# Performance work log

Hardware: AMD Instinct MI355X
Metric: run time of the kernel (lower is better)

## Reference

```python
import jax, jax.numpy as jnp
import numpy as np

B, S, D, H, L, F, V = 8, 4096, 1024, 16, 6, 2048, 256
DH = D // H

def _pe(seq, dim):
    pos = jnp.arange(seq, dtype=jnp.float32)[:, None]
    div = jnp.exp(jnp.arange(0, dim, 2, dtype=jnp.float32) * (-np.log(10000.0) / dim))
    pe = jnp.zeros((seq, dim), jnp.float32)
    pe = pe.at[:, 0::2].set(jnp.sin(pos * div))
    pe = pe.at[:, 1::2].set(jnp.cos(pos * div))
    return pe

def _ln(x, w, b):
    m = x.mean(-1, keepdims=True)
    v = ((x - m) ** 2).mean(-1, keepdims=True)
    return (x - m) * jax.lax.rsqrt(v + 1e-5) * w + b

def setup_inputs():
    key = jax.random.key(0)
    ks = jax.random.split(key, 8)
    s = 0.02
    return {
        'tgt': jax.random.normal(ks[0], (B, S, D), jnp.float32),
        'in_proj_w': jax.random.normal(ks[1], (L, 3 * D, D), jnp.float32) * s,
        'in_proj_b': jnp.zeros((L, 3 * D), jnp.float32),
        'out_proj_w': jax.random.normal(ks[2], (L, D, D), jnp.float32) * s,
        'out_proj_b': jnp.zeros((L, D), jnp.float32),
        'ln1_w': jnp.ones((L, D), jnp.float32), 'ln1_b': jnp.zeros((L, D), jnp.float32),
        'lin1_w': jax.random.normal(ks[3], (L, F, D), jnp.float32) * s,
        'lin1_b': jnp.zeros((L, F), jnp.float32),
        'lin2_w': jax.random.normal(ks[4], (L, D, F), jnp.float32) * s,
        'lin2_b': jnp.zeros((L, D), jnp.float32),
        'ln2_w': jnp.ones((L, D), jnp.float32), 'ln2_b': jnp.zeros((L, D), jnp.float32),
        'w_out': jax.random.normal(ks[5], (V, D), jnp.float32) * s,
        'b_out': jnp.zeros((V,), jnp.float32),
    }

def reference(tgt, in_proj_w, in_proj_b, out_proj_w, out_proj_b, ln1_w, ln1_b,
              lin1_w, lin1_b, lin2_w, lin2_b, ln2_w, ln2_b, w_out, b_out):
    # eval-mode cached decode step of CachedDecoderOnly.forward (dropout inactive)
    out = tgt + _pe(S, D)[None]  # [B,S,D]
    for i in range(L):
        q = out[:, -1:, :]  # query is only the last token
        wq, wk, wv = jnp.split(in_proj_w[i], 3, axis=0)
        bq, bk, bv = jnp.split(in_proj_b[i], 3)
        Q = (q @ wq.T + bq).reshape(B, 1, H, DH)
        K = (out @ wk.T + bk).reshape(B, -1, H, DH)
        Vv = (out @ wv.T + bv).reshape(B, -1, H, DH)
        sc = jnp.einsum('bqhd,bkhd->bhqk', Q, K) / jnp.sqrt(jnp.float32(DH))
        a = jax.nn.softmax(sc, axis=-1)
        o = jnp.einsum('bhqk,bkhd->bqhd', a, Vv).reshape(B, 1, D)
        o = o @ out_proj_w[i].T + out_proj_b[i]
        y = _ln(q + o, ln1_w[i], ln1_b[i])
        ff = jax.nn.relu(y @ lin1_w[i].T + lin1_b[i]) @ lin2_w[i].T + lin2_b[i]
        out = _ln(y + ff, ln2_w[i], ln2_b[i])  # [B,1,D] -> src for next layer
    return out @ w_out.T + b_out  # [B,1,V]
```

## Files before the change

### kernel.cpp

```cpp
#include <hip/hip_runtime.h>
#include <hip/hip_bf16.h>

#define BB 8
#define SS 4096
#define DD 1024
#define HH 16
#define LL 6
#define FF 2048
#define VV 256
#define NC 32

typedef __attribute__((ext_vector_type(8))) short bf16x8;
typedef __attribute__((ext_vector_type(4))) float f32x4;

__device__ __forceinline__ unsigned short f2bf(float f) {
    union { float f; unsigned u; } v; v.f = f;
    unsigned r = v.u + 0x7FFFu + ((v.u >> 16) & 1u);
    return (unsigned short)(r >> 16);
}

__global__ __launch_bounds__(256) void pe_kernel(float* __restrict__ pe) {
    int s = blockIdx.x;
    float fs = (float)s;
    for (int i = threadIdx.x; i < DD / 2; i += 256) {
        float div = expf((-logf(10000.0f) / (float)DD) * (float)(2 * i));
        float a = fs * div;
        pe[(long)s * DD + 2 * i]     = sinf(a);
        pe[(long)s * DD + 2 * i + 1] = cosf(a);
    }
}

template <int K, int RELU, int MODE>
__global__ __launch_bounds__(256) void gemm8k(
    const float* __restrict__ A, long sA,
    const float* __restrict__ A2, long sA2,
    const float* __restrict__ W,
    const float* __restrict__ bias,
    const float* __restrict__ R1, long sR1,
    const float* __restrict__ R2, long sR2,
    const float* __restrict__ lnw, const float* __restrict__ lnb,
    const float* __restrict__ lnsrc,
    float* __restrict__ C, int N)
{
    int wave = threadIdx.x >> 6, lane = threadIdx.x & 63;
    int n = blockIdx.x * 4 + wave;
    if (n >= N) return;

    float mean[8], rstd[8];
    if (MODE != 0) {
        const float* S = (MODE == 1) ? A : lnsrc;
        long ss = (MODE == 1) ? sA : 1024L;
        const int SK = (MODE == 1) ? K : 1024;
        #pragma unroll
        for (int m = 0; m < 8; ++m) {
            float s1 = 0.f, s2 = 0.f;
            const float4* Sr = reinterpret_cast<const float4*>(S + (long)m * ss);
            #pragma unroll
            for (int k4 = 0; k4 < SK / 256; ++k4) {
                float4 a = Sr[k4 * 64 + lane];
                s1 += a.x + a.y + a.z + a.w;
                s2 += a.x * a.x + a.y * a.y + a.z * a.z + a.w * a.w;
            }
            for (int off = 32; off; off >>= 1) {
                s1 += __shfl_xor(s1, off, 64);
                s2 += __shfl_xor(s2, off, 64);
            }
            float mu = s1 / (float)SK;
            mean[m] = mu;
            rstd[m] = rsqrtf(s2 / (float)SK - mu * mu + 1e-5f);
        }
    }

    float acc[8] = {0.f,0.f,0.f,0.f,0.f,0.f,0.f,0.f};
    const float4* W4 = reinterpret_cast<const float4*>(W + (long)n * K);
    float4 wv[K / 256];
    #pragma unroll
    for (int kb = 0; kb < K / 256; ++kb) wv[kb] = W4[kb * 64 + lane];
    #pragma unroll
    for (int kb = 0; kb < K / 256; ++kb) {
        int k4 = kb * 64 + lane;
        float4 w = wv[kb];
        float4 lw, lb;
        if (MODE == 1) {
            lw = reinterpret_cast<const float4*>(lnw)[k4];
            lb = reinterpret_cast<const float4*>(lnb)[k4];
        }
        #pragma unroll
        for (int m = 0; m < 8; ++m) {
            float4 a = reinterpret_cast<const float4*>(A + (long)m * sA)[k4];
            if (A2) {
                float4 a2 = reinterpret_cast<const float4*>(A2 + (long)m * sA2)[k4];
                a.x += a2.x; a.y += a2.y; a.z += a2.z; a.w += a2.w;
            }
            if (MODE == 1) {
                float mu = mean[m], rs = rstd[m];
                a.x = (a.x - mu) * rs * lw.x + lb.x;
                a.y = (a.y - mu) * rs * lw.y + lb.y;
                a.z = (a.z - mu) * rs * lw.z + lb.z;
                a.w = (a.w - mu) * rs * lw.w + lb.w;
            }
            acc[m] += a.x * w.x + a.y * w.y + a.z * w.z + a.w * w.w;
        }
    }
    #pragma unroll
    for (int m = 0; m < 8; ++m)
        for (int off = 32; off; off >>= 1) acc[m] += __shfl_xor(acc[m], off, 64);
    if (lane == 0) {
        float bs = bias ? bias[n] : 0.f;
        #pragma unroll
        for (int m = 0; m < 8; ++m) {
            float v = acc[m] + bs;
            if (MODE == 0) {
                if (R1) v += R1[(long)m * sR1 + n];
                if (R2) v += R2[(long)m * sR2 + n];
            }
            if (MODE == 2)
                v += (lnsrc[(long)m * 1024 + n] - mean[m]) * rstd[m] * lnw[n] + lnb[n];
            if (RELU) v = fmaxf(v, 0.f);
            C[(long)m * N + n] = v;
        }
    }
}

__global__ __launch_bounds__(256) void u_kernel(const float* __restrict__ Q,
                                                const float* __restrict__ wk,
                                                unsigned short* __restrict__ ub)
{
    int h = blockIdx.y;
    int e = blockIdx.x * 256 + threadIdx.x;
    __shared__ float qs[8][64];
    for (int idx = threadIdx.x; idx < 512; idx += 256) {
        int b = idx >> 6, d = idx & 63;
        qs[b][d] = Q[(long)b * DD + h * 64 + d];
    }
    __syncthreads();
    float acc[8] = {0.f,0.f,0.f,0.f,0.f,0.f,0.f,0.f};
    for (int d = 0; d < 64; ++d) {
        float wv = wk[(long)(h * 64 + d) * DD + e];
        #pragma unroll
        for (int b = 0; b < 8; ++b) acc[b] += qs[b][d] * wv;
    }
    #pragma unroll
    for (int b = 0; b < 8; ++b)
        ub[((long)(b * HH + h)) * DD + e] = f2bf(acc[b]);
}

__global__ __launch_bounds__(512) void attn_kernel(
    const float* __restrict__ tgt, const float* __restrict__ pe,
    const unsigned short* __restrict__ ub,
    float* __restrict__ ctxp, float* __restrict__ ml)
{
    int sc = blockIdx.x, b = blockIdx.y;
    int wave = threadIdx.x >> 6, lane = threadIdx.x & 63;
    int q = lane >> 4, n = lane & 15;
    __shared__ float scs[16][128];
    __shared__ unsigned short P[16 * 128];

    int s0 = sc * 128;

    {
        int s = s0 + wave * 16 + n;
        const float* xrow = tgt + ((long)b * SS + s) * DD;
        const float* prow = pe + (long)s * DD;
        const unsigned short* urow = ub + ((long)(b * HH) + n) * DD;
        f32x4 acc = {0.f, 0.f, 0.f, 0.f};
        #pragma unroll 4
        for (int ks = 0; ks < 32; ++ks) {
            int e0 = ks * 32 + q * 8;
            bf16x8 a = *reinterpret_cast<const bf16x8*>(urow + e0);
            float4 x0 = *reinterpret_cast<const float4*>(xrow + e0);
            float4 x1 = *reinterpret_cast<const float4*>(xrow + e0 + 4);
            float4 p0 = *reinterpret_cast<const float4*>(prow + e0);
            float4 p1 = *reinterpret_cast<const float4*>(prow + e0 + 4);
            union { short sh[8]; bf16x8 v; } bu;
            bu.sh[0] = (short)f2bf(x0.x + p0.x);
            bu.sh[1] = (short)f2bf(x0.y + p0.y);
            bu.sh[2] = (short)f2bf(x0.z + p0.z);
            bu.sh[3] = (short)f2bf(x0.w + p0.w);
            bu.sh[4] = (short)f2bf(x1.x + p1.x);
            bu.sh[5] = (short)f2bf(x1.y + p1.y);
            bu.sh[6] = (short)f2bf(x1.z + p1.z);
            bu.sh[7] = (short)f2bf(x1.w + p1.w);
            acc = __builtin_amdgcn_mfma_f32_16x16x32_bf16(a, bu.v, acc, 0, 0, 0);
        }
        #pragma unroll
        for (int r = 0; r < 4; ++r) scs[q * 4 + r][wave * 16 + n] = acc[r];
    }
    __syncthreads();

    {
        int h = threadIdx.x >> 5, l = threadIdx.x & 31;
        float4 v = *reinterpret_cast<const float4*>(&scs[h][l * 4]);
        v.x *= 0.125f; v.y *= 0.125f; v.z *= 0.125f; v.w *= 0.125f;
        float mx = fmaxf(fmaxf(v.x, v.y), fmaxf(v.z, v.w));
        #pragma unroll
        for (int off = 16; off; off >>= 1) mx = fmaxf(mx, __shfl_xor(mx, off, 32));
        float e0 = expf(v.x - mx), e1 = expf(v.y - mx);
        float e2 = expf(v.z - mx), e3 = expf(v.w - mx);
        float sum = e0 + e1 + e2 + e3;
        #pragma unroll
        for (int off = 16; off; off >>= 1) sum += __shfl_xor(sum, off, 32);
        unsigned d0 = (unsigned)f2bf(e0) | ((unsigned)f2bf(e1) << 16);
        unsigned d1 = (unsigned)f2bf(e2) | ((unsigned)f2bf(e3) << 16);
        char* Pb = reinterpret_cast<char*>(P);
        *reinterpret_cast<uint2*>(Pb + ((h * 256 + l * 8) ^ ((h & 7) << 4))) = make_uint2(d0, d1);
        if (l == 0) {
            long mi = ((long)sc * BB + b) * HH + h;
            ml[mi * 2] = mx;
            ml[mi * 2 + 1] = sum;
        }
    }
    __syncthreads();

    {
        const char* Pb = reinterpret_cast<const char*>(P);
        f32x4 cacc[8];
        #pragma unroll
        for (int t = 0; t < 8; ++t) cacc[t] = (f32x4){0.f, 0.f, 0.f, 0.f};
        #pragma unroll
        for (int ks2 = 0; ks2 < 4; ++ks2) {
            int sb = ks2 * 32 + q * 8;
            bf16x8 a = *reinterpret_cast<const bf16x8*>(
                Pb + ((n * 256 + sb * 2) ^ ((n & 7) << 4)));
            const float* xb  = tgt + ((long)b * SS + s0 + sb) * DD;
            const float* pb2 = pe + (long)(s0 + sb) * DD;
            #pragma unroll
            for (int t = 0; t < 8; ++t) {
                int e = wave * 128 + t * 16 + n;
                union { short sh[8]; bf16x8 v; } bu;
                #pragma unroll
                for (int j = 0; j < 8; ++j)
                    bu.sh[j] = (short)f2bf(xb[(long)j * DD + e] + pb2[(long)j * DD + e]);
                cacc[t] = __builtin_amdgcn_mfma_f32_16x16x32_bf16(a, bu.v, cacc[t], 0, 0, 0);
            }
        }
        long base = (((long)sc * BB + b) * HH) * DD;
        #pragma unroll
        for (int t = 0; t < 8; ++t) {
            int e = wave * 128 + t * 16 + n;
            #pragma unroll
            for (int r = 0; r < 4; ++r)
                ctxp[base + (long)(q * 4 + r) * DD + e] = cacc[t][r];
        }
    }
}

__global__ __launch_bounds__(256) void ctxred_kernel(const float* __restrict__ ctxp,
                                                     const float* __restrict__ ml,
                                                     float* __restrict__ ctx)
{
    int row = blockIdx.x;
    float M = -3.0e38f;
    #pragma unroll
    for (int c = 0; c < NC; ++c) M = fmaxf(M, ml[((long)c * BB * HH + row) * 2]);
    float L = 0.f;
    float scl[NC];
    #pragma unroll
    for (int c = 0; c < NC; ++c) {
        float e = expf(ml[((long)c * BB * HH + row) * 2] - M);
        scl[c] = e;
        L += e * ml[((long)c * BB * HH + row) * 2 + 1];
    }
    float inv = 1.f / L;
    int e4 = threadIdx.x * 4;
    float4 s = make_float4(0.f, 0.f, 0.f, 0.f);
    #pragma unroll
    for (int c = 0; c < NC; ++c) {
        float4 p = *reinterpret_cast<const float4*>(
            ctxp + ((long)c * BB * HH + row) * DD + e4);
        float f = scl[c];
        s.x += p.x * f; s.y += p.y * f; s.z += p.z * f; s.w += p.w * f;
    }
    s.x *= inv; s.y *= inv; s.z *= inv; s.w *= inv;
    *reinterpret_cast<float4*>(ctx + (long)row * DD + e4) = s;
}

__global__ __launch_bounds__(256) void ov_kernel(const float* __restrict__ ctx,
                                                 const float* __restrict__ wv,
                                                 const float* __restrict__ bv,
                                                 float* __restrict__ o)
{
    int wave = threadIdx.x >> 6, lane = threadIdx.x & 63;
    int j = blockIdx.x * 4 + wave;
    if (j >= DD) return;
    int h = j >> 6;
    float acc[8] = {0.f,0.f,0.f,0.f,0.f,0.f,0.f,0.f};
    const float4* w4 = reinterpret_cast<const float4*>(wv + (long)j * DD);
    float4 wreg[4];
    #pragma unroll
    for (int kb = 0; kb < 4; ++kb) wreg[kb] = w4[kb * 64 + lane];
    #pragma unroll
    for (int kb = 0; kb < 4; ++kb) {
        int k4 = kb * 64 + lane;
        float4 w = wreg[kb];
        #pragma unroll
        for (int b = 0; b < 8; ++b) {
            float4 a = reinterpret_cast<const float4*>(ctx + ((long)(b * HH + h)) * DD)[k4];
            acc[b] += a.x * w.x + a.y * w.y + a.z * w.z + a.w * w.w;
        }
    }
    #pragma unroll
    for (int b = 0; b < 8; ++b)
        for (int off = 32; off; off >>= 1) acc[b] += __shfl_xor(acc[b], off, 64);
    if (lane == 0) {
        float bs = bv[j];
        #pragma unroll
        for (int b = 0; b < 8; ++b) o[(long)b * DD + j] = acc[b] + bs;
    }
}

extern "C" void kernel_launch(void* const* d_in, const int* in_sizes, int n_in,
                              void* d_out, int out_size, void* d_ws, size_t ws_size,
                              hipStream_t stream)
{
    const float* tgt        = (const float*)d_in[0];
    const float* in_proj_w  = (const float*)d_in[1];
    const float* in_proj_b  = (const float*)d_in[2];
    const float* out_proj_w = (const float*)d_in[3];
    const float* out_proj_b = (const float*)d_in[4];
    const float* ln1_w      = (const float*)d_in[5];
    const float* ln1_b      = (const float*)d_in[6];
    const float* lin1_w     = (const float*)d_in[7];
    const float* lin1_b     = (const float*)d_in[8];
    const float* lin2_w     = (const float*)d_in[9];
    const float* lin2_b     = (const float*)d_in[10];
    const float* ln2_w      = (const float*)d_in[11];
    const float* ln2_b      = (const float*)d_in[12];
    const float* w_out      = (const float*)d_in[13];
    const float* b_out      = (const float*)d_in[14];

    float* ws = (float*)d_ws;
    long off = 0;
    float* pe   = ws + off;  off += (long)SS * DD;
    float* ctxp = ws + off;  off += (long)NC * BB * HH * DD;
    float* ml   = ws + off;  off += (long)NC * BB * HH * 2;
    float* ctx  = ws + off;  off += (long)BB * HH * DD;
    unsigned short* ub = (unsigned short*)(ws + off); off += (long)BB * HH * DD / 2;
    float* Q    = ws + off;  off += (long)BB * DD;
    float* o    = ws + off;  off += (long)BB * DD;
    float* vb   = ws + off;  off += (long)BB * DD;
    float* o2   = ws + off;  off += (long)BB * DD;
    float* hb   = ws + off;  off += (long)BB * FF;
    float* z    = ws + off;  off += (long)BB * DD;

    const float* tgt_last = tgt + (long)(SS - 1) * DD;
    const float* pe_last  = pe + (long)(SS - 1) * DD;

    pe_kernel<<<SS, 256, 0, stream>>>(pe);

    gemm8k<1024, 0, 0><<<DD / 4, 256, 0, stream>>>(
        tgt_last, (long)SS * DD, pe_last, 0L, in_proj_w, in_proj_b,
        nullptr, 0L, nullptr, 0L, nullptr, nullptr, nullptr, Q, DD);

    u_kernel<<<dim3(4, 16), 256, 0, stream>>>(Q, in_proj_w + (long)DD * DD, ub);

    attn_kernel<<<dim3(NC, BB), 512, 0, stream>>>(tgt, pe, ub, ctxp, ml);
    ctxred_kernel<<<BB * HH, 256, 0, stream>>>(ctxp, ml, ctx);

    ov_kernel<<<DD / 4, 256, 0, stream>>>(ctx, in_proj_w + 2L * DD * DD, in_proj_b + 2 * DD, o);

    gemm8k<1024, 0, 0><<<DD / 4, 256, 0, stream>>>(
        o, (long)DD, nullptr, 0L, out_proj_w, out_proj_b,
        tgt_last, (long)SS * DD, pe_last, 0L, nullptr, nullptr, nullptr, o2, DD);
    gemm8k<1024, 1, 1><<<FF / 4, 256, 0, stream>>>(
        o2, (long)DD, nullptr, 0L, lin1_w, lin1_b,
        nullptr, 0L, nullptr, 0L, ln1_w, ln1_b, nullptr, hb, FF);
    gemm8k<2048, 0, 2><<<DD / 4, 256, 0, stream>>>(
        hb, (long)FF, nullptr, 0L, lin2_w, lin2_b,
        nullptr, 0L, nullptr, 0L, ln1_w, ln1_b, o2, z, DD);

    for (int i = 1; i < LL; ++i) {
        const float* wv_i  = in_proj_w + (long)i * 3 * DD * DD + 2L * DD * DD;
        const float* bv_i  = in_proj_b + (long)i * 3 * DD + 2 * DD;
        const float* l2w_p = ln2_w + (long)(i - 1) * DD;
        const float* l2b_p = ln2_b + (long)(i - 1) * DD;
        const float* l1w   = ln1_w + (long)i * DD;
        const float* l1b   = ln1_b + (long)i * DD;
        gemm8k<1024, 0, 1><<<DD / 4, 256, 0, stream>>>(
            z, (long)DD, nullptr, 0L, wv_i, bv_i,
            nullptr, 0L, nullptr, 0L, l2w_p, l2b_p, nullptr, vb, DD);
        gemm8k<1024, 0, 2><<<DD / 4, 256, 0, stream>>>(
            vb, (long)DD, nullptr, 0L,
            out_proj_w + (long)i * DD * DD, out_proj_b + (long)i * DD,
            nullptr, 0L, nullptr, 0L, l2w_p, l2b_p, z, o2, DD);
        gemm8k<1024, 1, 1><<<FF / 4, 256, 0, stream>>>(
            o2, (long)DD, nullptr, 0L,
            lin1_w + (long)i * FF * DD, lin1_b + (long)i * FF,
            nullptr, 0L, nullptr, 0L, l1w, l1b, nullptr, hb, FF);
        gemm8k<2048, 0, 2><<<DD / 4, 256, 0, stream>>>(
            hb, (long)FF, nullptr, 0L,
            lin2_w + (long)i * DD * FF, lin2_b + (long)i * DD,
            nullptr, 0L, nullptr, 0L, l1w, l1b, o2, z, DD);
    }

    gemm8k<1024, 0, 1><<<VV / 4, 256, 0, stream>>>(
        z, (long)DD, nullptr, 0L, w_out, b_out,
        nullptr, 0L, nullptr, 0L,
        ln2_w + (long)(LL - 1) * DD, ln2_b + (long)(LL - 1) * DD, nullptr,
        (float*)d_out, VV);
}
```

Measured before the change: 614.6 us.

## Split-K across wave pairs in GEMV kernels, finer attention chunks, faster PE generation

Each gemm8k and ov_kernel block now uses 512 threads, with two waves per output column each handling half of K. Their partial sums are combined through shared memory, and the LayerNorm statistics are also split across two waves. This doubles the number of waves in flight on these latency-bound GEMVs. The attention kernel uses 64 chunks of 64 tokens, with the score MFMA split over two K-halves, and ctxred now runs as a 2D grid with a shuffle-based scale computation. pe_kernel computes 8 rows per block using the angle-addition recurrence, trading some float rounding drift for fewer sin/cos calls. Costs include extra shared-memory syncs and larger ctxp partial buffers.

```diff
diff --git a/kernel.cpp b/kernel.cpp
--- a/kernel.cpp
+++ b/kernel.cpp
@@ -8,7 +8,7 @@
 #define LL 6
 #define FF 2048
 #define VV 256
-#define NC 32
+#define NC 64
 
 typedef __attribute__((ext_vector_type(8))) short bf16x8;
 typedef __attribute__((ext_vector_type(4))) float f32x4;
@@ -20,18 +20,24 @@
 }
 
 __global__ __launch_bounds__(256) void pe_kernel(float* __restrict__ pe) {
-    int s = blockIdx.x;
-    float fs = (float)s;
+    int s0 = blockIdx.x * 8;
     for (int i = threadIdx.x; i < DD / 2; i += 256) {
         float div = expf((-logf(10000.0f) / (float)DD) * (float)(2 * i));
-        float a = fs * div;
-        pe[(long)s * DD + 2 * i]     = sinf(a);
-        pe[(long)s * DD + 2 * i + 1] = cosf(a);
+        float a0 = (float)s0 * div;
+        float sa = sinf(a0), ca = cosf(a0);
+        float sd = sinf(div), cd = cosf(div);
+        #pragma unroll
+        for (int r = 0; r < 8; ++r) {
+            reinterpret_cast<float2*>(pe + (long)(s0 + r) * DD)[i] = make_float2(sa, ca);
+            float sn = sa * cd + ca * sd;
+            ca = ca * cd - sa * sd;
+            sa = sn;
+        }
     }
 }
 
 template <int K, int RELU, int MODE>
-__global__ __launch_bounds__(256) void gemm8k(
+__global__ __launch_bounds__(512) void gemm8k(
     const float* __restrict__ A, long sA,
     const float* __restrict__ A2, long sA2,
     const float* __restrict__ W,
@@ -43,43 +49,59 @@
     float* __restrict__ C, int N)
 {
     int wave = threadIdx.x >> 6, lane = threadIdx.x & 63;
-    int n = blockIdx.x * 4 + wave;
-    if (n >= N) return;
+    int c = wave >> 1, kh = wave & 1;
+    int n = blockIdx.x * 4 + c;
+    constexpr int KH = K / 2;
+
+    __shared__ float stat[2][8][2];
+    __shared__ float part[8][8];
 
     float mean[8], rstd[8];
     if (MODE != 0) {
         const float* S = (MODE == 1) ? A : lnsrc;
         long ss = (MODE == 1) ? sA : 1024L;
-        const int SK = (MODE == 1) ? K : 1024;
+        constexpr int SK = (MODE == 1) ? K : 1024;
+        constexpr int SKH = SK / 2;
+        if (wave < 2) {
+            #pragma unroll
+            for (int m = 0; m < 8; ++m) {
+                float s1 = 0.f, s2 = 0.f;
+                const float4* Sr = reinterpret_cast<const float4*>(S + (long)m * ss) + kh * (SKH / 4);
+                #pragma unroll
+                for (int k4 = 0; k4 < SKH / 256; ++k4) {
+                    float4 a = Sr[k4 * 64 + lane];
+                    s1 += a.x + a.y + a.z + a.w;
+                    s2 += a.x * a.x + a.y * a.y + a.z * a.z + a.w * a.w;
+                }
+                #pragma unroll
+                for (int off = 32; off; off >>= 1) {
+                    s1 += __shfl_xor(s1, off, 64);
+                    s2 += __shfl_xor(s2, off, 64);
+                }
+                if (lane == 0) { stat[kh][m][0] = s1; stat[kh][m][1] = s2; }
+            }
+        }
+        __syncthreads();
+        constexpr float rSK = 1.f / (float)SK;
         #pragma unroll
         for (int m = 0; m < 8; ++m) {
-            float s1 = 0.f, s2 = 0.f;
-            const float4* Sr = reinterpret_cast<const float4*>(S + (long)m * ss);
-            #pragma unroll
-            for (int k4 = 0; k4 < SK / 256; ++k4) {
-                float4 a = Sr[k4 * 64 + lane];
-                s1 += a.x + a.y + a.z + a.w;
-                s2 += a.x * a.x + a.y * a.y + a.z * a.z + a.w * a.w;
-            }
-            for (int off = 32; off; off >>= 1) {
-                s1 += __shfl_xor(s1, off, 64);
-                s2 += __shfl_xor(s2, off, 64);
-            }
-            float mu = s1 / (float)SK;
+            float s1 = stat[0][m][0] + stat[1][m][0];
+            float s2 = stat[0][m][1] + stat[1][m][1];
+            float mu = s1 * rSK;
             mean[m] = mu;
-            rstd[m] = rsqrtf(s2 / (float)SK - mu * mu + 1e-5f);
+            rstd[m] = rsqrtf(s2 * rSK - mu * mu + 1e-5f);
         }
     }
 
     float acc[8] = {0.f,0.f,0.f,0.f,0.f,0.f,0.f,0.f};
-    const float4* W4 = reinterpret_cast<const float4*>(W + (long)n * K);
-    float4 wv[K / 256];
-    #pragma unroll
-    for (int kb = 0; kb < K / 256; ++kb) wv[kb] = W4[kb * 64 + lane];
-    #pragma unroll
-    for (int kb = 0; kb < K / 256; ++kb) {
-        int k4 = kb * 64 + lane;
-        float4 w = wv[kb];
+    const float4* W4 = reinterpret_cast<const float4*>(W + (long)n * K) + kh * (KH / 4);
+    float4 wreg[KH / 256];
+    #pragma unroll
+    for (int kb = 0; kb < KH / 256; ++kb) wreg[kb] = W4[kb * 64 + lane];
+    #pragma unroll
+    for (int kb = 0; kb < KH / 256; ++kb) {
+        int k4 = kh * (KH / 4) + kb * 64 + lane;
+        float4 w = wreg[kb];
         float4 lw, lb;
         if (MODE == 1) {
             lw = reinterpret_cast<const float4*>(lnw)[k4];
@@ -103,22 +125,26 @@
         }
     }
     #pragma unroll
-    for (int m = 0; m < 8; ++m)
+    for (int m = 0; m < 8; ++m) {
+        #pragma unroll
         for (int off = 32; off; off >>= 1) acc[m] += __shfl_xor(acc[m], off, 64);
+    }
     if (lane == 0) {
-        float bs = bias ? bias[n] : 0.f;
-        #pragma unroll
-        for (int m = 0; m < 8; ++m) {
-            float v = acc[m] + bs;
-            if (MODE == 0) {
-                if (R1) v += R1[(long)m * sR1 + n];
-                if (R2) v += R2[(long)m * sR2 + n];
-            }
-            if (MODE == 2)
-                v += (lnsrc[(long)m * 1024 + n] - mean[m]) * rstd[m] * lnw[n] + lnb[n];
-            if (RELU) v = fmaxf(v, 0.f);
-            C[(long)m * N + n] = v;
-        }
+        #pragma unroll
+        for (int m = 0; m < 8; ++m) part[wave][m] = acc[m];
+    }
+    __syncthreads();
+    if (kh == 0 && lane < 8) {
+        int m = lane;
+        float v = part[wave][m] + part[wave + 1][m] + (bias ? bias[n] : 0.f);
+        if (MODE == 0) {
+            if (R1) v += R1[(long)m * sR1 + n];
+            if (R2) v += R2[(long)m * sR2 + n];
+        }
+        if (MODE == 2)
+            v += (lnsrc[(long)m * 1024 + n] - mean[m]) * rstd[m] * lnw[n] + lnb[n];
+        if (RELU) v = fmaxf(v, 0.f);
+        C[(long)m * N + n] = v;
     }
 }
 
@@ -153,19 +179,20 @@
     int sc = blockIdx.x, b = blockIdx.y;
     int wave = threadIdx.x >> 6, lane = threadIdx.x & 63;
     int q = lane >> 4, n = lane & 15;
-    __shared__ float scs[16][128];
-    __shared__ unsigned short P[16 * 128];
-
-    int s0 = sc * 128;
+    __shared__ float scs[2][16][66];
+    __shared__ unsigned short P[16 * 64];
+
+    int s0 = sc * 64;
 
     {
-        int s = s0 + wave * 16 + n;
-        const float* xrow = tgt + ((long)b * SS + s) * DD;
-        const float* prow = pe + (long)s * DD;
-        const unsigned short* urow = ub + ((long)(b * HH) + n) * DD;
+        int st = wave >> 1, kh = wave & 1;
+        int s = s0 + st * 16 + n;
+        const float* xrow = tgt + ((long)b * SS + s) * DD + kh * 512;
+        const float* prow = pe + (long)s * DD + kh * 512;
+        const unsigned short* urow = ub + ((long)(b * HH) + n) * DD + kh * 512;
         f32x4 acc = {0.f, 0.f, 0.f, 0.f};
         #pragma unroll 4
-        for (int ks = 0; ks < 32; ++ks) {
+        for (int ks = 0; ks < 16; ++ks) {
             int e0 = ks * 32 + q * 8;
             bf16x8 a = *reinterpret_cast<const bf16x8*>(urow + e0);
             float4 x0 = *reinterpret_cast<const float4*>(xrow + e0);
@@ -184,26 +211,26 @@
             acc = __builtin_amdgcn_mfma_f32_16x16x32_bf16(a, bu.v, acc, 0, 0, 0);
         }
         #pragma unroll
-        for (int r = 0; r < 4; ++r) scs[q * 4 + r][wave * 16 + n] = acc[r];
+        for (int r = 0; r < 4; ++r) scs[kh][q * 4 + r][st * 16 + n] = acc[r];
     }
     __syncthreads();
 
     {
         int h = threadIdx.x >> 5, l = threadIdx.x & 31;
-        float4 v = *reinterpret_cast<const float4*>(&scs[h][l * 4]);
-        v.x *= 0.125f; v.y *= 0.125f; v.z *= 0.125f; v.w *= 0.125f;
-        float mx = fmaxf(fmaxf(v.x, v.y), fmaxf(v.z, v.w));
+        float2 v0 = *reinterpret_cast<const float2*>(&scs[0][h][l * 2]);
+        float2 v1 = *reinterpret_cast<const float2*>(&scs[1][h][l * 2]);
+        float a0 = (v0.x + v1.x) * 0.125f;
+        float a1 = (v0.y + v1.y) * 0.125f;
+        float mx = fmaxf(a0, a1);
         #pragma unroll
         for (int off = 16; off; off >>= 1) mx = fmaxf(mx, __shfl_xor(mx, off, 32));
-        float e0 = expf(v.x - mx), e1 = expf(v.y - mx);
-        float e2 = expf(v.z - mx), e3 = expf(v.w - mx);
-        float sum = e0 + e1 + e2 + e3;
+        float e0 = expf(a0 - mx), e1 = expf(a1 - mx);
+        float sum = e0 + e1;
         #pragma unroll
         for (int off = 16; off; off >>= 1) sum += __shfl_xor(sum, off, 32);
         unsigned d0 = (unsigned)f2bf(e0) | ((unsigned)f2bf(e1) << 16);
-        unsigned d1 = (unsigned)f2bf(e2) | ((unsigned)f2bf(e3) << 16);
         char* Pb = reinterpret_cast<char*>(P);
-        *reinterpret_cast<uint2*>(Pb + ((h * 256 + l * 8) ^ ((h & 7) << 4))) = make_uint2(d0, d1);
+        *reinterpret_cast<unsigned*>(Pb + ((h * 128 + l * 4) ^ ((h & 7) << 4))) = d0;
         if (l == 0) {
             long mi = ((long)sc * BB + b) * HH + h;
             ml[mi * 2] = mx;
@@ -218,10 +245,10 @@
         #pragma unroll
         for (int t = 0; t < 8; ++t) cacc[t] = (f32x4){0.f, 0.f, 0.f, 0.f};
         #pragma unroll
-        for (int ks2 = 0; ks2 < 4; ++ks2) {
+        for (int ks2 = 0; ks2 < 2; ++ks2) {
             int sb = ks2 * 32 + q * 8;
             bf16x8 a = *reinterpret_cast<const bf16x8*>(
-                Pb + ((n * 256 + sb * 2) ^ ((n & 7) << 4)));
+                Pb + ((n * 128 + sb * 2) ^ ((n & 7) << 4)));
             const float* xb  = tgt + ((long)b * SS + s0 + sb) * DD;
             const float* pb2 = pe + (long)(s0 + sb) * DD;
             #pragma unroll
@@ -250,48 +277,47 @@
                                                      float* __restrict__ ctx)
 {
     int row = blockIdx.x;
-    float M = -3.0e38f;
-    #pragma unroll
-    for (int c = 0; c < NC; ++c) M = fmaxf(M, ml[((long)c * BB * HH + row) * 2]);
-    float L = 0.f;
-    float scl[NC];
-    #pragma unroll
-    for (int c = 0; c < NC; ++c) {
-        float e = expf(ml[((long)c * BB * HH + row) * 2] - M);
-        scl[c] = e;
-        L += e * ml[((long)c * BB * HH + row) * 2 + 1];
-    }
-    float inv = 1.f / L;
-    int e4 = threadIdx.x * 4;
-    float4 s = make_float4(0.f, 0.f, 0.f, 0.f);
-    #pragma unroll
-    for (int c = 0; c < NC; ++c) {
-        float4 p = *reinterpret_cast<const float4*>(
-            ctxp + ((long)c * BB * HH + row) * DD + e4);
-        float f = scl[c];
-        s.x += p.x * f; s.y += p.y * f; s.z += p.z * f; s.w += p.w * f;
-    }
-    s.x *= inv; s.y *= inv; s.z *= inv; s.w *= inv;
-    *reinterpret_cast<float4*>(ctx + (long)row * DD + e4) = s;
-}
-
-__global__ __launch_bounds__(256) void ov_kernel(const float* __restrict__ ctx,
+    __shared__ float scl[NC];
+    int t = threadIdx.x;
+    if (t < 64) {
+        float m = ml[((long)t * BB * HH + row) * 2];
+        float l = ml[((long)t * BB * HH + row) * 2 + 1];
+        float M = m;
+        #pragma unroll
+        for (int off = 32; off; off >>= 1) M = fmaxf(M, __shfl_xor(M, off, 64));
+        float e = expf(m - M);
+        float L = e * l;
+        #pragma unroll
+        for (int off = 32; off; off >>= 1) L += __shfl_xor(L, off, 64);
+        scl[t] = e / L;
+    }
+    __syncthreads();
+    int e = blockIdx.y * 256 + t;
+    float s = 0.f;
+    #pragma unroll 8
+    for (int c = 0; c < NC; ++c)
+        s += scl[c] * ctxp[((long)c * BB * HH + row) * DD + e];
+    ctx[(long)row * DD + e] = s;
+}
+
+__global__ __launch_bounds__(512) void ov_kernel(const float* __restrict__ ctx,
                                                  const float* __restrict__ wv,
                                                  const float* __restrict__ bv,
                                                  float* __restrict__ o)
 {
     int wave = threadIdx.x >> 6, lane = threadIdx.x & 63;
-    int j = blockIdx.x * 4 + wave;
-    if (j >= DD) return;
+    int c = wave >> 1, kh = wave & 1;
+    int j = blockIdx.x * 4 + c;
     int h = j >> 6;
+    __shared__ float part[8][8];
     float acc[8] = {0.f,0.f,0.f,0.f,0.f,0.f,0.f,0.f};
-    const float4* w4 = reinterpret_cast<const float4*>(wv + (long)j * DD);
-    float4 wreg[4];
-    #pragma unroll
-    for (int kb = 0; kb < 4; ++kb) wreg[kb] = w4[kb * 64 + lane];
-    #pragma unroll
-    for (int kb = 0; kb < 4; ++kb) {
-        int k4 = kb * 64 + lane;
+    const float4* w4 = reinterpret_cast<const float4*>(wv + (long)j * DD) + kh * 128;
+    float4 wreg[2];
+    #pragma unroll
+    for (int kb = 0; kb < 2; ++kb) wreg[kb] = w4[kb * 64 + lane];
+    #pragma unroll
+    for (int kb = 0; kb < 2; ++kb) {
+        int k4 = kh * 128 + kb * 64 + lane;
         float4 w = wreg[kb];
         #pragma unroll
         for (int b = 0; b < 8; ++b) {
@@ -300,12 +326,18 @@
         }
     }
     #pragma unroll
-    for (int b = 0; b < 8; ++b)
+    for (int b = 0; b < 8; ++b) {
+        #pragma unroll
         for (int off = 32; off; off >>= 1) acc[b] += __shfl_xor(acc[b], off, 64);
+    }
     if (lane == 0) {
-        float bs = bv[j];
-        #pragma unroll
-        for (int b = 0; b < 8; ++b) o[(long)b * DD + j] = acc[b] + bs;
+        #pragma unroll
+        for (int b = 0; b < 8; ++b) part[wave][b] = acc[b];
+    }
+    __syncthreads();
+    if (kh == 0 && lane < 8) {
+        int b = lane;
+        o[(long)b * DD + j] = part[wave][b] + part[wave + 1][b] + bv[j];
     }
 }
 
@@ -346,26 +378,26 @@
     const float* tgt_last = tgt + (long)(SS - 1) * DD;
     const float* pe_last  = pe + (long)(SS - 1) * DD;
 
-    pe_kernel<<<SS, 256, 0, stream>>>(pe);
-
-    gemm8k<1024, 0, 0><<<DD / 4, 256, 0, stream>>>(
+    pe_kernel<<<SS / 8, 256, 0, stream>>>(pe);
+
+    gemm8k<1024, 0, 0><<<DD / 4, 512, 0, stream>>>(
         tgt_last, (long)SS * DD, pe_last, 0L, in_proj_w, in_proj_b,
         nullptr, 0L, nullptr, 0L, nullptr, nullptr, nullptr, Q, DD);
 
     u_kernel<<<dim3(4, 16), 256, 0, stream>>>(Q, in_proj_w + (long)DD * DD, ub);
 
     attn_kernel<<<dim3(NC, BB), 512, 0, stream>>>(tgt, pe, ub, ctxp, ml);
-    ctxred_kernel<<<BB * HH, 256, 0, stream>>>(ctxp, ml, ctx);
-
-    ov_kernel<<<DD / 4, 256, 0, stream>>>(ctx, in_proj_w + 2L * DD * DD, in_proj_b + 2 * DD, o);
-
-    gemm8k<1024, 0, 0><<<DD / 4, 256, 0, stream>>>(
+    ctxred_kernel<<<dim3(BB * HH, 4), 256, 0, stream>>>(ctxp, ml, ctx);
+
+    ov_kernel<<<DD / 4, 512, 0, stream>>>(ctx, in_proj_w + 2L * DD * DD, in_proj_b + 2 * DD, o);
+
+    gemm8k<1024, 0, 0><<<DD / 4, 512, 0, stream>>>(
         o, (long)DD, nullptr, 0L, out_proj_w, out_proj_b,
         tgt_last, (long)SS * DD, pe_last, 0L, nullptr, nullptr, nullptr, o2, DD);
-    gemm8k<1024, 1, 1><<<FF / 4, 256, 0, stream>>>(
+    gemm8k<1024, 1, 1><<<FF / 4, 512, 0, stream>>>(
         o2, (long)DD, nullptr, 0L, lin1_w, lin1_b,
         nullptr, 0L, nullptr, 0L, ln1_w, ln1_b, nullptr, hb, FF);
-    gemm8k<2048, 0, 2><<<DD / 4, 256, 0, stream>>>(
+    gemm8k<2048, 0, 2><<<DD / 4, 512, 0, stream>>>(
         hb, (long)FF, nullptr, 0L, lin2_w, lin2_b,
         nullptr, 0L, nullptr, 0L, ln1_w, ln1_b, o2, z, DD);
 
@@ -376,24 +408,24 @@
         const float* l2b_p = ln2_b + (long)(i - 1) * DD;
         const float* l1w   = ln1_w + (long)i * DD;
         const float* l1b   = ln1_b + (long)i * DD;
-        gemm8k<1024, 0, 1><<<DD / 4, 256, 0, stream>>>(
+        gemm8k<1024, 0, 1><<<DD / 4, 512, 0, stream>>>(
             z, (long)DD, nullptr, 0L, wv_i, bv_i,
             nullptr, 0L, nullptr, 0L, l2w_p, l2b_p, nullptr, vb, DD);
-        gemm8k<1024, 0, 2><<<DD / 4, 256, 0, stream>>>(
+        gemm8k<1024, 0, 2><<<DD / 4, 512, 0, stream>>>(
             vb, (long)DD, nullptr, 0L,
             out_proj_w + (long)i * DD * DD, out_proj_b + (long)i * DD,
             nullptr, 0L, nullptr, 0L, l2w_p, l2b_p, z, o2, DD);
-        gemm8k<1024, 1, 1><<<FF / 4, 256, 0, stream>>>(
+        gemm8k<1024, 1, 1><<<FF / 4, 512, 0, stream>>>(
             o2, (long)DD, nullptr, 0L,
             lin1_w + (long)i * FF * DD, lin1_b + (long)i * FF,
             nullptr, 0L, nullptr, 0L, l1w, l1b, nullptr, hb, FF);
-        gemm8k<2048, 0, 2><<<DD / 4, 256, 0, stream>>>(
+        gemm8k<2048, 0, 2><<<DD / 4, 512, 0, stream>>>(
             hb, (long)FF, nullptr, 0L,
             lin2_w + (long)i * DD * FF, lin2_b + (long)i * DD,
             nullptr, 0L, nullptr, 0L, l1w, l1b, o2, z, DD);
     }
 
-    gemm8k<1024, 0, 1><<<VV / 4, 256, 0, stream>>>(
+    gemm8k<1024, 0, 1><<<VV / 4, 512, 0, stream>>>(
         z, (long)DD, nullptr, 0L, w_out, b_out,
         nullptr, 0L, nullptr, 0L,
         ln2_w + (long)(LL - 1) * DD, ln2_b + (long)(LL - 1) * DD, nullptr,
```

Measured after the change: 633.2 us. 3.0% more time.

## Precompute bf16 x+PE once and halve attention chunk size

Applied to the files above, without the earlier changes.

A new prep kernel adds the positional encoding to tgt once and stores the sum as bf16, using an angle-addition recurrence in place of per-element sin/cos. The attention kernel then reads this bf16 buffer for both the score and context MMAs instead of fp32 tgt plus fp32 pe, halving its read traffic. Chunks shrink from 128 to 64 tokens, giving twice the blocks and splitting K across waves. The reduction kernel is reworked with a wave-level max/sum and a 2D grid. The trade-off is an extra full pass that writes a 64MB bf16 copy, and the recurrence can slightly change PE precision.

```diff
diff --git a/kernel.cpp b/kernel.cpp
--- a/kernel.cpp
+++ b/kernel.cpp
@@ -8,7 +8,7 @@
 #define LL 6
 #define FF 2048
 #define VV 256
-#define NC 32
+#define NC 64
 
 typedef __attribute__((ext_vector_type(8))) short bf16x8;
 typedef __attribute__((ext_vector_type(4))) float f32x4;
@@ -19,14 +19,33 @@
     return (unsigned short)(r >> 16);
 }
 
-__global__ __launch_bounds__(256) void pe_kernel(float* __restrict__ pe) {
-    int s = blockIdx.x;
-    float fs = (float)s;
+__global__ __launch_bounds__(256) void pelast_kernel(float* __restrict__ pl) {
     for (int i = threadIdx.x; i < DD / 2; i += 256) {
         float div = expf((-logf(10000.0f) / (float)DD) * (float)(2 * i));
-        float a = fs * div;
-        pe[(long)s * DD + 2 * i]     = sinf(a);
-        pe[(long)s * DD + 2 * i + 1] = cosf(a);
+        float a = (float)(SS - 1) * div;
+        pl[2 * i]     = sinf(a);
+        pl[2 * i + 1] = cosf(a);
+    }
+}
+
+__global__ __launch_bounds__(256) void xprep_kernel(const float* __restrict__ tgt,
+                                                    unsigned* __restrict__ xb)
+{
+    int s0 = blockIdx.x * 8, b = blockIdx.y;
+    for (int i = threadIdx.x; i < DD / 2; i += 256) {
+        float div = expf((-logf(10000.0f) / (float)DD) * (float)(2 * i));
+        float a0 = (float)s0 * div;
+        float sa = sinf(a0), ca = cosf(a0);
+        float sd = sinf(div), cd = cosf(div);
+        #pragma unroll
+        for (int r = 0; r < 8; ++r) {
+            float2 t = reinterpret_cast<const float2*>(tgt + ((long)b * SS + s0 + r) * DD)[i];
+            unsigned lo = f2bf(t.x + sa), hi = f2bf(t.y + ca);
+            xb[((long)b * SS + s0 + r) * (DD / 2) + i] = lo | (hi << 16);
+            float sn = sa * cd + ca * sd;
+            ca = ca * cd - sa * sd;
+            sa = sn;
+        }
     }
 }
 
@@ -145,65 +164,53 @@
         ub[((long)(b * HH + h)) * DD + e] = f2bf(acc[b]);
 }
 
-__global__ __launch_bounds__(512) void attn_kernel(
-    const float* __restrict__ tgt, const float* __restrict__ pe,
+__global__ __launch_bounds__(512, 4) void attn_kernel(
+    const unsigned short* __restrict__ xb,
     const unsigned short* __restrict__ ub,
     float* __restrict__ ctxp, float* __restrict__ ml)
 {
     int sc = blockIdx.x, b = blockIdx.y;
     int wave = threadIdx.x >> 6, lane = threadIdx.x & 63;
     int q = lane >> 4, n = lane & 15;
-    __shared__ float scs[16][128];
-    __shared__ unsigned short P[16 * 128];
-
-    int s0 = sc * 128;
+    __shared__ float scs[2][16][66];
+    __shared__ unsigned short P[16 * 64];
+
+    int s0 = sc * 64;
 
     {
-        int s = s0 + wave * 16 + n;
-        const float* xrow = tgt + ((long)b * SS + s) * DD;
-        const float* prow = pe + (long)s * DD;
-        const unsigned short* urow = ub + ((long)(b * HH) + n) * DD;
+        int st = wave >> 1, kh = wave & 1;
+        int s = s0 + st * 16 + n;
+        const unsigned short* xrow = xb + ((long)b * SS + s) * DD + kh * 512;
+        const unsigned short* urow = ub + ((long)(b * HH) + n) * DD + kh * 512;
         f32x4 acc = {0.f, 0.f, 0.f, 0.f};
-        #pragma unroll 4
-        for (int ks = 0; ks < 32; ++ks) {
+        #pragma unroll
+        for (int ks = 0; ks < 16; ++ks) {
             int e0 = ks * 32 + q * 8;
-            bf16x8 a = *reinterpret_cast<const bf16x8*>(urow + e0);
-            float4 x0 = *reinterpret_cast<const float4*>(xrow + e0);
-            float4 x1 = *reinterpret_cast<const float4*>(xrow + e0 + 4);
-            float4 p0 = *reinterpret_cast<const float4*>(prow + e0);
-            float4 p1 = *reinterpret_cast<const float4*>(prow + e0 + 4);
-            union { short sh[8]; bf16x8 v; } bu;
-            bu.sh[0] = (short)f2bf(x0.x + p0.x);
-            bu.sh[1] = (short)f2bf(x0.y + p0.y);
-            bu.sh[2] = (short)f2bf(x0.z + p0.z);
-            bu.sh[3] = (short)f2bf(x0.w + p0.w);
-            bu.sh[4] = (short)f2bf(x1.x + p1.x);
-            bu.sh[5] = (short)f2bf(x1.y + p1.y);
-            bu.sh[6] = (short)f2bf(x1.z + p1.z);
-            bu.sh[7] = (short)f2bf(x1.w + p1.w);
-            acc = __builtin_amdgcn_mfma_f32_16x16x32_bf16(a, bu.v, acc, 0, 0, 0);
-        }
-        #pragma unroll
-        for (int r = 0; r < 4; ++r) scs[q * 4 + r][wave * 16 + n] = acc[r];
+            bf16x8 a  = *reinterpret_cast<const bf16x8*>(urow + e0);
+            bf16x8 xv = *reinterpret_cast<const bf16x8*>(xrow + e0);
+            acc = __builtin_amdgcn_mfma_f32_16x16x32_bf16(a, xv, acc, 0, 0, 0);
+        }
+        #pragma unroll
+        for (int r = 0; r < 4; ++r) scs[kh][q * 4 + r][st * 16 + n] = acc[r];
     }
     __syncthreads();
 
     {
         int h = threadIdx.x >> 5, l = threadIdx.x & 31;
-        float4 v = *reinterpret_cast<const float4*>(&scs[h][l * 4]);
-        v.x *= 0.125f; v.y *= 0.125f; v.z *= 0.125f; v.w *= 0.125f;
-        float mx = fmaxf(fmaxf(v.x, v.y), fmaxf(v.z, v.w));
+        float2 v0 = *reinterpret_cast<const float2*>(&scs[0][h][l * 2]);
+        float2 v1 = *reinterpret_cast<const float2*>(&scs[1][h][l * 2]);
+        float a0 = (v0.x + v1.x) * 0.125f;
+        float a1 = (v0.y + v1.y) * 0.125f;
+        float mx = fmaxf(a0, a1);
         #pragma unroll
         for (int off = 16; off; off >>= 1) mx = fmaxf(mx, __shfl_xor(mx, off, 32));
-        float e0 = expf(v.x - mx), e1 = expf(v.y - mx);
-        float e2 = expf(v.z - mx), e3 = expf(v.w - mx);
-        float sum = e0 + e1 + e2 + e3;
+        float e0 = expf(a0 - mx), e1 = expf(a1 - mx);
+        float sum = e0 + e1;
         #pragma unroll
         for (int off = 16; off; off >>= 1) sum += __shfl_xor(sum, off, 32);
         unsigned d0 = (unsigned)f2bf(e0) | ((unsigned)f2bf(e1) << 16);
-        unsigned d1 = (unsigned)f2bf(e2) | ((unsigned)f2bf(e3) << 16);
         char* Pb = reinterpret_cast<char*>(P);
-        *reinterpret_cast<uint2*>(Pb + ((h * 256 + l * 8) ^ ((h & 7) << 4))) = make_uint2(d0, d1);
+        *reinterpret_cast<unsigned*>(Pb + ((h * 128 + l * 4) ^ ((h & 7) << 4))) = d0;
         if (l == 0) {
             long mi = ((long)sc * BB + b) * HH + h;
             ml[mi * 2] = mx;
@@ -214,24 +221,28 @@
 
     {
         const char* Pb = reinterpret_cast<const char*>(P);
+        bf16x8 pa[2];
+        #pragma unroll
+        for (int ks2 = 0; ks2 < 2; ++ks2) {
+            int sb = ks2 * 32 + q * 8;
+            pa[ks2] = *reinterpret_cast<const bf16x8*>(
+                Pb + ((n * 128 + sb * 2) ^ ((n & 7) << 4)));
+        }
         f32x4 cacc[8];
         #pragma unroll
         for (int t = 0; t < 8; ++t) cacc[t] = (f32x4){0.f, 0.f, 0.f, 0.f};
         #pragma unroll
-        for (int ks2 = 0; ks2 < 4; ++ks2) {
+        for (int ks2 = 0; ks2 < 2; ++ks2) {
             int sb = ks2 * 32 + q * 8;
-            bf16x8 a = *reinterpret_cast<const bf16x8*>(
-                Pb + ((n * 256 + sb * 2) ^ ((n & 7) << 4)));
-            const float* xb  = tgt + ((long)b * SS + s0 + sb) * DD;
-            const float* pb2 = pe + (long)(s0 + sb) * DD;
+            const unsigned short* xbase = xb + ((long)b * SS + s0 + sb) * DD;
             #pragma unroll
             for (int t = 0; t < 8; ++t) {
                 int e = wave * 128 + t * 16 + n;
-                union { short sh[8]; bf16x8 v; } bu;
+                union { unsigned short sh[8]; bf16x8 v; } bu;
                 #pragma unroll
                 for (int j = 0; j < 8; ++j)
-                    bu.sh[j] = (short)f2bf(xb[(long)j * DD + e] + pb2[(long)j * DD + e]);
-                cacc[t] = __builtin_amdgcn_mfma_f32_16x16x32_bf16(a, bu.v, cacc[t], 0, 0, 0);
+                    bu.sh[j] = xbase[(long)j * DD + e];
+                cacc[t] = __builtin_amdgcn_mfma_f32_16x16x32_bf16(pa[ks2], bu.v, cacc[t], 0, 0, 0);
             }
         }
         long base = (((long)sc * BB + b) * HH) * DD;
@@ -250,29 +261,27 @@
                                                      float* __restrict__ ctx)
 {
     int row = blockIdx.x;
-    float M = -3.0e38f;
-    #pragma unroll
-    for (int c = 0; c < NC; ++c) M = fmaxf(M, ml[((long)c * BB * HH + row) * 2]);
-    float L = 0.f;
-    float scl[NC];
-    #pragma unroll
-    for (int c = 0; c < NC; ++c) {
-        float e = expf(ml[((long)c * BB * HH + row) * 2] - M);
-        scl[c] = e;
-        L += e * ml[((long)c * BB * HH + row) * 2 + 1];
-    }
-    float inv = 1.f / L;
-    int e4 = threadIdx.x * 4;
-    float4 s = make_float4(0.f, 0.f, 0.f, 0.f);
-    #pragma unroll
-    for (int c = 0; c < NC; ++c) {
-        float4 p = *reinterpret_cast<const float4*>(
-            ctxp + ((long)c * BB * HH + row) * DD + e4);
-        float f = scl[c];
-        s.x += p.x * f; s.y += p.y * f; s.z += p.z * f; s.w += p.w * f;
-    }
-    s.x *= inv; s.y *= inv; s.z *= inv; s.w *= inv;
-    *reinterpret_cast<float4*>(ctx + (long)row * DD + e4) = s;
+    __shared__ float scl[NC];
+    int t = threadIdx.x;
+    if (t < 64) {
+        float m = ml[((long)t * BB * HH + row) * 2];
+        float l = ml[((long)t * BB * HH + row) * 2 + 1];
+        float M = m;
+        #pragma unroll
+        for (int off = 32; off; off >>= 1) M = fmaxf(M, __shfl_xor(M, off, 64));
+        float e = expf(m - M);
+        float L = e * l;
+        #pragma unroll
+        for (int off = 32; off; off >>= 1) L += __shfl_xor(L, off, 64);
+        scl[t] = e / L;
+    }
+    __syncthreads();
+    int e = blockIdx.y * 256 + t;
+    float s = 0.f;
+    #pragma unroll 8
+    for (int c = 0; c < NC; ++c)
+        s += scl[c] * ctxp[((long)c * BB * HH + row) * DD + e];
+    ctx[(long)row * DD + e] = s;
 }
 
 __global__ __launch_bounds__(256) void ov_kernel(const float* __restrict__ ctx,
@@ -331,11 +340,12 @@
 
     float* ws = (float*)d_ws;
     long off = 0;
-    float* pe   = ws + off;  off += (long)SS * DD;
+    unsigned short* xb = (unsigned short*)(ws + off); off += (long)BB * SS * DD / 2;
     float* ctxp = ws + off;  off += (long)NC * BB * HH * DD;
     float* ml   = ws + off;  off += (long)NC * BB * HH * 2;
     float* ctx  = ws + off;  off += (long)BB * HH * DD;
     unsigned short* ub = (unsigned short*)(ws + off); off += (long)BB * HH * DD / 2;
+    float* pl   = ws + off;  off += DD;
     float* Q    = ws + off;  off += (long)BB * DD;
     float* o    = ws + off;  off += (long)BB * DD;
     float* vb   = ws + off;  off += (long)BB * DD;
@@ -344,24 +354,24 @@
     float* z    = ws + off;  off += (long)BB * DD;
 
     const float* tgt_last = tgt + (long)(SS - 1) * DD;
-    const float* pe_last  = pe + (long)(SS - 1) * DD;
-
-    pe_kernel<<<SS, 256, 0, stream>>>(pe);
+
+    pelast_kernel<<<1, 256, 0, stream>>>(pl);
+    xprep_kernel<<<dim3(SS / 8, BB), 256, 0, stream>>>(tgt, (unsigned*)xb);
 
     gemm8k<1024, 0, 0><<<DD / 4, 256, 0, stream>>>(
-        tgt_last, (long)SS * DD, pe_last, 0L, in_proj_w, in_proj_b,
+        tgt_last, (long)SS * DD, pl, 0L, in_proj_w, in_proj_b,
         nullptr, 0L, nullptr, 0L, nullptr, nullptr, nullptr, Q, DD);
 
     u_kernel<<<dim3(4, 16), 256, 0, stream>>>(Q, in_proj_w + (long)DD * DD, ub);
 
-    attn_kernel<<<dim3(NC, BB), 512, 0, stream>>>(tgt, pe, ub, ctxp, ml);
-    ctxred_kernel<<<BB * HH, 256, 0, stream>>>(ctxp, ml, ctx);
+    attn_kernel<<<dim3(NC, BB), 512, 0, stream>>>(xb, ub, ctxp, ml);
+    ctxred_kernel<<<dim3(BB * HH, 4), 256, 0, stream>>>(ctxp, ml, ctx);
 
     ov_kernel<<<DD / 4, 256, 0, stream>>>(ctx, in_proj_w + 2L * DD * DD, in_proj_b + 2 * DD, o);
 
     gemm8k<1024, 0, 0><<<DD / 4, 256, 0, stream>>>(
         o, (long)DD, nullptr, 0L, out_proj_w, out_proj_b,
-        tgt_last, (long)SS * DD, pe_last, 0L, nullptr, nullptr, nullptr, o2, DD);
+        tgt_last, (long)SS * DD, pl, 0L, nullptr, nullptr, nullptr, o2, DD);
     gemm8k<1024, 1, 1><<<FF / 4, 256, 0, stream>>>(
         o2, (long)DD, nullptr, 0L, lin1_w, lin1_b,
         nullptr, 0L, nullptr, 0L, ln1_w, ln1_b, nullptr, hb, FF);
```

Measured after the change: 611.5 us. About the same (-0.5%).
